# Kernel optimization log

Measured on AMD Instinct MI355X. Metric: run time of the kernel, lower is better.

## Reference

```python
import jax, jax.numpy as jnp
import numpy as np

B, T, D = 4, 2048, 768
H = 12
HD = D // H
WINDOW = 128

def setup_inputs() -> dict:
    key = jax.random.key(0)
    k1, k2, k3 = jax.random.split(key, 3)
    x = jax.random.normal(k1, (B, T, D), dtype=jnp.float32)
    Wqkv = jax.random.normal(k2, (D, 3 * D), dtype=jnp.float32) * 0.02
    Wout = jax.random.normal(k3, (D, D), dtype=jnp.float32) * 0.02
    return {"x": x, "Wqkv": Wqkv, "Wout": Wout}

def reference(x, Wqkv, Wout):
    Bx, Tx, Dx = x.shape
    qkv = x @ Wqkv                      # [B,T,3D]
    q, k, v = jnp.split(qkv, 3, axis=-1)
    def heads(t):
        return t.reshape(Bx, Tx, H, HD).transpose(0, 2, 1, 3)  # [B,H,T,hd]
    q, k, v = heads(q), heads(k), heads(v)
    scale = 1.0 / jnp.sqrt(jnp.float32(HD))
    scores = jnp.einsum('bhqd,bhkd->bhqk', q, k) * scale       # [B,H,T,T]
    pos = jnp.arange(Tx)
    dist = pos[None, :] - pos[:, None]                          # j - i
    blocked = (dist > 0) | (dist < -WINDOW)                     # causal band
    scores = jnp.where(blocked[None, None], -jnp.inf, scores)
    attn = jax.nn.softmax(scores, axis=-1)
    out = jnp.einsum('bhqk,bhkd->bhqd', attn, v)                # [B,H,T,hd]
    out = out.transpose(0, 2, 1, 3).reshape(Bx, Tx, Dx)
    return out @ Wout
```

## Files before the change

### kernel.cpp

```cpp
#include <hip/hip_runtime.h>
#include <hip/hip_bf16.h>
#include <stdint.h>

typedef unsigned short u16;
typedef __attribute__((ext_vector_type(8))) short short8;
typedef __attribute__((ext_vector_type(8))) __bf16 bf16x8;
typedef __attribute__((ext_vector_type(4))) float f32x4;

constexpr int Bc  = 4;
constexpr int Tc  = 2048;
constexpr int Dc  = 768;
constexpr int Hc  = 12;
constexpr int WINc = 128;

static __device__ __forceinline__ u16 f2bf(float f) {
  union { float f; uint32_t u; } v; v.f = f;
  uint32_t u = v.u;
  return (u16)((u + 0x7fffu + ((u >> 16) & 1u)) >> 16);
}

static __device__ __forceinline__ f32x4 mfma16x16x32(bf16x8 a, bf16x8 b, f32x4 c) {
  return __builtin_amdgcn_mfma_f32_16x16x32_bf16(a, b, c, 0, 0, 0);
}

#define GLOAD_LDS16(gsrc, ldst)                                                \
  __builtin_amdgcn_global_load_lds(                                            \
      (const __attribute__((address_space(1))) void*)(gsrc),                   \
      (__attribute__((address_space(3))) void*)(ldst), 16, 0, 0)

__global__ __launch_bounds__(256) void cvt_f32_to_bf16(const float* __restrict__ in,
                                                       u16* __restrict__ out) {
  const int i = blockIdx.x * 256 + threadIdx.x;
  const float4 f = ((const float4*)in)[i];
  union { u16 h[4]; uint2 u; } pk;
  pk.h[0] = f2bf(f.x); pk.h[1] = f2bf(f.y); pk.h[2] = f2bf(f.z); pk.h[3] = f2bf(f.w);
  ((uint2*)out)[i] = pk.u;
}

__global__ __launch_bounds__(256) void transpose_cvt(const float* __restrict__ W,
                                                     u16* __restrict__ WT,
                                                     int R, int C) {
  __shared__ float tile[64][65];
  const int t  = threadIdx.x;
  const int c0 = blockIdx.x * 64, r0 = blockIdx.y * 64;
#pragma unroll
  for (int i = 0; i < 16; ++i) {
    const int e = i * 256 + t;
    const int r = e >> 6, c = e & 63;
    tile[r][c] = W[(size_t)(r0 + r) * C + c0 + c];
  }
  __syncthreads();
#pragma unroll
  for (int i = 0; i < 16; ++i) {
    const int e = i * 256 + t;
    const int r = e >> 6, c = e & 63;
    WT[(size_t)(c0 + r) * R + r0 + c] = f2bf(tile[c][r]);
  }
}

template <int EPI>
__global__ __launch_bounds__(256) void gemm_bt(const u16* __restrict__ A,
                                               const u16* __restrict__ Bt,
                                               u16* __restrict__ q_ws,
                                               u16* __restrict__ k_ws,
                                               u16* __restrict__ v_ws,
                                               float* __restrict__ fout) {
  __shared__ u16 As[128][32];
  __shared__ u16 Bs[128][32];
  const int t  = threadIdx.x;
  const int w  = t >> 6, l = t & 63;
  const int lr = l & 15, lh = l >> 4;
  const int wm = w >> 1, wn = w & 1;
  const int m0 = blockIdx.y * 128, n0 = blockIdx.x * 128;

  f32x4 acc[4][4];
#pragma unroll
  for (int mi = 0; mi < 4; ++mi)
#pragma unroll
    for (int ni = 0; ni < 4; ++ni) acc[mi][ni] = f32x4{0.f, 0.f, 0.f, 0.f};

  const int srow = l >> 2;
  const int scol = (l & 3) * 8;
  const u16* aP = A  + (size_t)(m0 + w * 16 + srow) * 768 + scol;
  const u16* bP = Bt + (size_t)(n0 + w * 16 + srow) * 768 + scol;
  char* asB = (char*)As + w * 1024;
  char* bsB = (char*)Bs + w * 1024;

  for (int kt = 0; kt < 24; ++kt) {
    const int ko = kt * 32;
    __syncthreads();
    GLOAD_LDS16(aP + ko,            asB);
    GLOAD_LDS16(aP + ko + 64 * 768, asB + 4096);
    GLOAD_LDS16(bP + ko,            bsB);
    GLOAD_LDS16(bP + ko + 64 * 768, bsB + 4096);
    __syncthreads();

    bf16x8 af[4], bfr[4];
#pragma unroll
    for (int mi = 0; mi < 4; ++mi)
      af[mi] = *(const bf16x8*)&As[wm * 64 + mi * 16 + lr][lh * 8];
#pragma unroll
    for (int ni = 0; ni < 4; ++ni)
      bfr[ni] = *(const bf16x8*)&Bs[wn * 64 + ni * 16 + lr][lh * 8];
#pragma unroll
    for (int mi = 0; mi < 4; ++mi)
#pragma unroll
      for (int ni = 0; ni < 4; ++ni)
        acc[mi][ni] = mfma16x16x32(af[mi], bfr[ni], acc[mi][ni]);
  }

  if (EPI == 0) {
#pragma unroll
    for (int mi = 0; mi < 4; ++mi)
#pragma unroll
      for (int ni = 0; ni < 4; ++ni) {
        const int col   = n0 + wn * 64 + ni * 16 + lr;
        const int which = col / 768;
        const int rem   = col - which * 768;
        const int h     = rem >> 6, d = rem & 63;
        u16* dst = (which == 0) ? q_ws : ((which == 1) ? k_ws : v_ws);
#pragma unroll
        for (int r = 0; r < 4; ++r) {
          const int m  = m0 + wm * 64 + mi * 16 + lh * 4 + r;
          const int bb = m >> 11, tt = m & 2047;
          dst[(((size_t)(bb * Hc + h) * Tc + tt) << 6) + d] = f2bf(acc[mi][ni][r]);
        }
      }
  } else {
#pragma unroll
    for (int mi = 0; mi < 4; ++mi)
#pragma unroll
      for (int ni = 0; ni < 4; ++ni) {
        const int col = n0 + wn * 64 + ni * 16 + lr;
#pragma unroll
        for (int r = 0; r < 4; ++r) {
          const int m = m0 + wm * 64 + mi * 16 + lh * 4 + r;
          fout[(size_t)m * 768 + col] = acc[mi][ni][r];
        }
      }
  }
}

__global__ __launch_bounds__(256) void swa_attn(const u16* __restrict__ Q,
                                                const u16* __restrict__ Kk,
                                                const u16* __restrict__ V,
                                                u16* __restrict__ Out) {
  __shared__ u16 Qs[64][72];
  __shared__ u16 Ks[64][72];
  __shared__ u16 Vt[64][72];
  __shared__ u16 Ps[4][16][72];

  const int t  = threadIdx.x;
  const int w  = t >> 6, l = t & 63;
  const int lr = l & 15, lh = l >> 4;
  const int bh = blockIdx.y;
  const int q0 = blockIdx.x * 64;
  const size_t head_base = (size_t)bh * Tc * 64;

  {
    const int row = t >> 2, c = (t & 3) * 16;
    const short8* src = (const short8*)(Q + head_base + (size_t)(q0 + row) * 64 + c);
    *(short8*)&Qs[row][c]     = src[0];
    *(short8*)&Qs[row][c + 8] = src[1];
  }

  float m_r[4], l_r[4];
  f32x4 Oa[4];
#pragma unroll
  for (int r = 0; r < 4; ++r) { m_r[r] = -1e30f; l_r[r] = 0.f; }
#pragma unroll
  for (int n = 0; n < 4; ++n) Oa[n] = f32x4{0.f, 0.f, 0.f, 0.f};

  const int kb_lo = (q0 >= WINc) ? q0 - WINc : 0;
  for (int kb = kb_lo; kb <= q0; kb += 64) {
    __syncthreads();
    {
      const int row = t >> 2, c = (t & 3) * 16;
      const short8* ksrc = (const short8*)(Kk + head_base + (size_t)(kb + row) * 64 + c);
      *(short8*)&Ks[row][c]     = ksrc[0];
      *(short8*)&Ks[row][c + 8] = ksrc[1];
      const short8* vsrc = (const short8*)(V + head_base + (size_t)(kb + row) * 64 + c);
      short8 v0 = vsrc[0], v1 = vsrc[1];
#pragma unroll
      for (int j = 0; j < 8; ++j) {
        Vt[c + j][row]     = (u16)v0[j];
        Vt[c + 8 + j][row] = (u16)v1[j];
      }
    }
    __syncthreads();

    bf16x8 qa0 = *(const bf16x8*)&Qs[w * 16 + lr][lh * 8];
    bf16x8 qa1 = *(const bf16x8*)&Qs[w * 16 + lr][32 + lh * 8];

    f32x4 s[4];
#pragma unroll
    for (int sub = 0; sub < 4; ++sub) {
      bf16x8 kb0 = *(const bf16x8*)&Ks[sub * 16 + lr][lh * 8];
      bf16x8 kb1 = *(const bf16x8*)&Ks[sub * 16 + lr][32 + lh * 8];
      f32x4 z = f32x4{0.f, 0.f, 0.f, 0.f};
      z = mfma16x16x32(qa0, kb0, z);
      z = mfma16x16x32(qa1, kb1, z);
      s[sub] = z;
    }

    const int qbase = q0 + w * 16 + lh * 4;
#pragma unroll
    for (int sub = 0; sub < 4; ++sub) {
      const int kj = kb + sub * 16 + lr;
#pragma unroll
      for (int r = 0; r < 4; ++r) {
        const int qi = qbase + r;
        const bool ok = (kj <= qi) && (kj + WINc >= qi);
        s[sub][r] = ok ? s[sub][r] * 0.125f : -1e30f;
      }
    }

    float mt[4];
#pragma unroll
    for (int r = 0; r < 4; ++r)
      mt[r] = fmaxf(fmaxf(s[0][r], s[1][r]), fmaxf(s[2][r], s[3][r]));
#pragma unroll
    for (int msk = 1; msk < 16; msk <<= 1)
#pragma unroll
      for (int r = 0; r < 4; ++r)
        mt[r] = fmaxf(mt[r], __shfl_xor(mt[r], msk, 64));

    float al[4];
#pragma unroll
    for (int r = 0; r < 4; ++r) {
      const float mn = fmaxf(m_r[r], mt[r]);
      al[r] = __expf(m_r[r] - mn);
      m_r[r] = mn;
    }

    float rs[4] = {0.f, 0.f, 0.f, 0.f};
#pragma unroll
    for (int sub = 0; sub < 4; ++sub)
#pragma unroll
      for (int r = 0; r < 4; ++r) {
        const float p = __expf(s[sub][r] - m_r[r]);
        s[sub][r] = p;
        rs[r] += p;
      }
#pragma unroll
    for (int msk = 1; msk < 16; msk <<= 1)
#pragma unroll
      for (int r = 0; r < 4; ++r)
        rs[r] += __shfl_xor(rs[r], msk, 64);
#pragma unroll
    for (int r = 0; r < 4; ++r) l_r[r] = l_r[r] * al[r] + rs[r];

#pragma unroll
    for (int n = 0; n < 4; ++n)
#pragma unroll
      for (int r = 0; r < 4; ++r) Oa[n][r] *= al[r];

#pragma unroll
    for (int sub = 0; sub < 4; ++sub)
#pragma unroll
      for (int r = 0; r < 4; ++r)
        Ps[w][lh * 4 + r][sub * 16 + lr] = f2bf(s[sub][r]);

#pragma unroll
    for (int ks = 0; ks < 2; ++ks) {
      bf16x8 pa = *(const bf16x8*)&Ps[w][lr][ks * 32 + lh * 8];
#pragma unroll
      for (int n = 0; n < 4; ++n) {
        bf16x8 vb = *(const bf16x8*)&Vt[n * 16 + lr][ks * 32 + lh * 8];
        Oa[n] = mfma16x16x32(pa, vb, Oa[n]);
      }
    }
  }

  const int bb = bh / Hc, h = bh - bb * Hc;
#pragma unroll
  for (int n = 0; n < 4; ++n)
#pragma unroll
    for (int r = 0; r < 4; ++r) {
      const float val = Oa[n][r] / l_r[r];
      const int ti = q0 + w * 16 + lh * 4 + r;
      Out[((size_t)(bb * Tc + ti)) * 768 + h * 64 + n * 16 + lr] = f2bf(val);
    }
}

extern "C" void kernel_launch(void* const* d_in, const int* in_sizes, int n_in,
                              void* d_out, int out_size, void* d_ws, size_t ws_size,
                              hipStream_t stream) {
  (void)in_sizes; (void)n_in; (void)out_size; (void)ws_size;
  const float* x    = (const float*)d_in[0];
  const float* Wqkv = (const float*)d_in[1];
  const float* Wout = (const float*)d_in[2];
  float* out = (float*)d_out;

  u16* ws    = (u16*)d_ws;
  u16* xb    = ws;
  u16* wqkvT = xb + 6291456;
  u16* woutT = wqkvT + 1769472;
  u16* qws   = woutT + 589824;
  u16* kws   = qws + 6291456;
  u16* vws   = kws + 6291456;
  u16* aws   = xb;

  cvt_f32_to_bf16<<<6144, 256, 0, stream>>>(x, xb);
  transpose_cvt<<<dim3(36, 12), 256, 0, stream>>>(Wqkv, wqkvT, 768, 2304);
  transpose_cvt<<<dim3(12, 12), 256, 0, stream>>>(Wout, woutT, 768, 768);
  gemm_bt<0><<<dim3(18, 64), 256, 0, stream>>>(xb, wqkvT, qws, kws, vws, nullptr);
  swa_attn<<<dim3(32, 48), 256, 0, stream>>>(qws, kws, vws, aws);
  gemm_bt<1><<<dim3(6, 64), 256, 0, stream>>>(aws, woutT, nullptr, nullptr, nullptr, out);
}
```

Before: 113.6 us.

## Widen GEMM K-tile to 64 with XOR-swizzled LDS and fold softmax scale into Q

The projection GEMM now stages 64-wide K tiles per iteration, which halves the number of k-loop iterations and barrier pairs. The LDS columns use an XOR swizzle on 16-byte chunks to avoid bank conflicts on the fragment reads. The 1/sqrt(hd) scale moves into the Q epilogue of the QKV GEMM, so the attention kernel drops a multiply per score. Doubling the shared-memory footprint may lower occupancy, and rounding Q to bf16 after scaling by 0.125 is exact because it is a power of two.

```diff
diff --git a/kernel.cpp b/kernel.cpp
--- a/kernel.cpp
+++ b/kernel.cpp
@@ -65,8 +65,8 @@
                                                u16* __restrict__ k_ws,
                                                u16* __restrict__ v_ws,
                                                float* __restrict__ fout) {
-  __shared__ u16 As[128][32];
-  __shared__ u16 Bs[128][32];
+  __shared__ u16 As[128][64];
+  __shared__ u16 Bs[128][64];
   const int t  = threadIdx.x;
   const int w  = t >> 6, l = t & 63;
   const int lr = l & 15, lh = l >> 4;
@@ -79,34 +79,39 @@
 #pragma unroll
     for (int ni = 0; ni < 4; ++ni) acc[mi][ni] = f32x4{0.f, 0.f, 0.f, 0.f};
 
-  const int srow = l >> 2;
-  const int scol = (l & 3) * 8;
-  const u16* aP = A  + (size_t)(m0 + w * 16 + srow) * 768 + scol;
-  const u16* bP = Bt + (size_t)(n0 + w * 16 + srow) * 768 + scol;
+  const int srow = w * 8 + (l >> 3);
+  const int scol = ((l & 7) ^ (l >> 3)) * 8;
+  const u16* aP = A  + (size_t)(m0 + srow) * 768 + scol;
+  const u16* bP = Bt + (size_t)(n0 + srow) * 768 + scol;
   char* asB = (char*)As + w * 1024;
   char* bsB = (char*)Bs + w * 1024;
 
-  for (int kt = 0; kt < 24; ++kt) {
-    const int ko = kt * 32;
+  for (int kt = 0; kt < 12; ++kt) {
+    const int ko = kt * 64;
     __syncthreads();
-    GLOAD_LDS16(aP + ko,            asB);
-    GLOAD_LDS16(aP + ko + 64 * 768, asB + 4096);
-    GLOAD_LDS16(bP + ko,            bsB);
-    GLOAD_LDS16(bP + ko + 64 * 768, bsB + 4096);
+#pragma unroll
+    for (int j = 0; j < 4; ++j) {
+      GLOAD_LDS16(aP + ko + j * (32 * 768), asB + j * 4096);
+      GLOAD_LDS16(bP + ko + j * (32 * 768), bsB + j * 4096);
+    }
     __syncthreads();
 
-    bf16x8 af[4], bfr[4];
-#pragma unroll
-    for (int mi = 0; mi < 4; ++mi)
-      af[mi] = *(const bf16x8*)&As[wm * 64 + mi * 16 + lr][lh * 8];
-#pragma unroll
-    for (int ni = 0; ni < 4; ++ni)
-      bfr[ni] = *(const bf16x8*)&Bs[wn * 64 + ni * 16 + lr][lh * 8];
-#pragma unroll
-    for (int mi = 0; mi < 4; ++mi)
+#pragma unroll
+    for (int kk = 0; kk < 2; ++kk) {
+      const int cb = (kk * 64 + lh * 16) ^ ((lr & 7) << 4);
+      bf16x8 af[4], bfr[4];
+#pragma unroll
+      for (int mi = 0; mi < 4; ++mi)
+        af[mi] = *(const bf16x8*)((const char*)As + (wm * 64 + mi * 16 + lr) * 128 + cb);
 #pragma unroll
       for (int ni = 0; ni < 4; ++ni)
-        acc[mi][ni] = mfma16x16x32(af[mi], bfr[ni], acc[mi][ni]);
+        bfr[ni] = *(const bf16x8*)((const char*)Bs + (wn * 64 + ni * 16 + lr) * 128 + cb);
+#pragma unroll
+      for (int mi = 0; mi < 4; ++mi)
+#pragma unroll
+        for (int ni = 0; ni < 4; ++ni)
+          acc[mi][ni] = mfma16x16x32(af[mi], bfr[ni], acc[mi][ni]);
+    }
   }
 
   if (EPI == 0) {
@@ -119,11 +124,12 @@
         const int rem   = col - which * 768;
         const int h     = rem >> 6, d = rem & 63;
         u16* dst = (which == 0) ? q_ws : ((which == 1) ? k_ws : v_ws);
+        const float scl = (which == 0) ? 0.125f : 1.0f;
 #pragma unroll
         for (int r = 0; r < 4; ++r) {
           const int m  = m0 + wm * 64 + mi * 16 + lh * 4 + r;
           const int bb = m >> 11, tt = m & 2047;
-          dst[(((size_t)(bb * Hc + h) * Tc + tt) << 6) + d] = f2bf(acc[mi][ni][r]);
+          dst[(((size_t)(bb * Hc + h) * Tc + tt) << 6) + d] = f2bf(acc[mi][ni][r] * scl);
         }
       }
   } else {
@@ -211,7 +217,7 @@
       for (int r = 0; r < 4; ++r) {
         const int qi = qbase + r;
         const bool ok = (kj <= qi) && (kj + WINc >= qi);
-        s[sub][r] = ok ? s[sub][r] * 0.125f : -1e30f;
+        s[sub][r] = ok ? s[sub][r] : -1e30f;
       }
     }
 
```

Measured after the change: 110.7 us. 1.03x faster.
